# Kernel tuning notes

Measured on AMD Instinct MI355X. Metric: run time of the kernel, lower is better.

## Reference

```python
import jax, jax.numpy as jnp
import numpy as np

# Static module config (matches init_kwargs)
K = 9            # kernel_size for piecewise-linear basis with kernel_shape (3,4)
GROUPS = 1
NLAT_IN, NLON_IN = 361, 720
NLAT_OUT, NLON_OUT = 181, 360
NNZ = 120000


def _disco_s2_contraction(x, ker_idx, row_idx, col_idx, vals):
    """Sparse DISCO contraction: y[b,c,k,ho,wo] = sum_e [ker_e=k][row_e=ho]
    vals_e * x[b,c,hi_e,(wi_e + wo*pscale) % nlon_in].
    Implemented as a longitude-roll scan with gather + segment_sum (no dense psi)."""
    B, C, Hi, Wi = x.shape
    pscale = Wi // NLON_OUT
    hi = col_idx // Wi          # [nnz] input latitude
    wi = col_idx % Wi           # [nnz] input longitude (unshifted)
    seg = ker_idx * NLAT_OUT + row_idx  # [nnz] output (k, ho) segment id

    def step(x_c, _):
        # gather all nnz entries for the current longitude shift: [nnz, B*C]
        g = x_c[:, :, hi, wi].reshape(B * C, -1).T
        y = jax.ops.segment_sum(g * vals[:, None], seg, num_segments=K * NLAT_OUT)
        # roll so next output longitude sees x[..., (wi + pscale) % Wi]
        return jnp.roll(x_c, -pscale, axis=-1), y

    _, ys = jax.lax.scan(step, x, None, length=NLON_OUT)  # [Wo, K*Ho, B*C]
    y = jnp.transpose(ys, (2, 1, 0)).reshape(B, C, K, NLAT_OUT, NLON_OUT)
    return y


def setup_inputs() -> dict:
    key = jax.random.key(0)
    k1, k2, k3, k4, k5, k6, k7 = jax.random.split(key, 7)
    B, Cin, Cout = 1, 32, 32
    x = jax.random.normal(k1, (B, Cin, NLAT_IN, NLON_IN), dtype=jnp.float32)
    psi_ker_idx = jax.random.randint(k2, (NNZ,), 0, K)
    psi_row_idx = jax.random.randint(k3, (NNZ,), 0, NLAT_OUT)
    psi_col_idx = jax.random.randint(k4, (NNZ,), 0, NLAT_IN * NLON_IN)
    psi_vals = jax.random.normal(k5, (NNZ,), dtype=jnp.float32) * 0.05
    groupsize = Cin // GROUPS
    scale = np.sqrt(1.0 / groupsize)
    weight = scale * jax.random.normal(k6, (Cout, groupsize, K), dtype=jnp.float32)
    bias = jax.random.normal(k7, (Cout,), dtype=jnp.float32) * 0.01
    return {"x": x, "psi_ker_idx": psi_ker_idx, "psi_row_idx": psi_row_idx,
            "psi_col_idx": psi_col_idx, "psi_vals": psi_vals,
            "weight": weight, "bias": bias}


def reference(x, psi_ker_idx, psi_row_idx, psi_col_idx, psi_vals, weight, bias):
    # sparse gather-weight-scatter contraction -> [B, C, K, Ho, Wo]
    xk = _disco_s2_contraction(x, psi_ker_idx, psi_row_idx, psi_col_idx, psi_vals)
    B, C, _, H, W = xk.shape
    groupsize = C // GROUPS
    xk = xk.reshape(B, GROUPS, groupsize, K, H, W)
    w = weight.reshape(GROUPS, -1, weight.shape[1], weight.shape[2])  # [g, o, c, k]
    out = jnp.einsum('bgckxy,gock->bgoxy', xk, w).reshape(B, -1, H, W)
    out = out + bias.reshape(1, -1, 1, 1)
    return out
```

## Files before the change

### kernel.cpp

```cpp
#include <hip/hip_runtime.h>
#include <hip/hip_bf16.h>
#include <stdint.h>

typedef uint32_t u32;
typedef unsigned short u16;
typedef float v2f __attribute__((ext_vector_type(2)));

#define NLAT_I 361
#define NLON_I 720
#define NLAT_O 181
#define NLON_O 360
#define KK 9
#define NNZ 120000
#define NSEG (KK * NLAT_O)
#define NPIX (NLAT_O * NLON_O)
#define NCH 32
#define SORT_CAP 512
#define ROWLEN 5760

#define NBLK1 233
#define SEGS_PER_BLK 7
#define NC 8
#define LDSCAP 160
#define SPIN_LIMIT 100

__device__ __forceinline__ u32 f2bf_rne(float f) {
    u32 b = __float_as_uint(f);
    return (b + 0x7FFFu + ((b >> 16) & 1u)) >> 16;
}

__global__ __launch_bounds__(256) void repack_kernel(const float* __restrict__ x,
                                                     u32* __restrict__ xp) {
    __shared__ u16 tile[32][732];
    int hi = blockIdx.x;
    int tid = threadIdx.x;
    const size_t plane = (size_t)NLAT_I * NLON_I;
#pragma unroll 1
    for (int c = 0; c < NCH; c++) {
        for (int col = tid; col < NLON_I; col += 256) {
            tile[c][col] = (u16)f2bf_rne(x[c * plane + (size_t)hi * NLON_I + col]);
        }
    }
    __syncthreads();
    for (int wdx = tid; wdx < 2 * ROWLEN; wdx += 256) {
        int p = wdx / ROWLEN;
        int rem = wdx - p * ROWLEN;
        int j = rem >> 4;
        int cp = rem & 15;
        int col = 2 * j + p;
        u32 v = (u32)tile[2 * cp][col] | ((u32)tile[2 * cp + 1][col] << 16);
        xp[(size_t)(2 * hi + p) * ROWLEN + rem] = v;
    }
}

__global__ __launch_bounds__(256) void hist_kernel(const int* __restrict__ ker,
                                                   const int* __restrict__ row,
                                                   int* __restrict__ counts) {
    int e = blockIdx.x * 256 + threadIdx.x;
    if (e >= NNZ) return;
    int seg = ker[e] * NLAT_O + row[e];
    atomicAdd(&counts[seg], 1);
}

__global__ __launch_bounds__(256) void scan_kernel(const int* __restrict__ counts,
                                                   int* __restrict__ offsets) {
    __shared__ int lsum[256];
    const int CH = 7;
    int t = threadIdx.x;
    int base = t * CH;
    int local[CH];
    int s = 0;
    for (int i = 0; i < CH; i++) {
        int v = (base + i < NSEG) ? counts[base + i] : 0;
        local[i] = s;
        s += v;
    }
    lsum[t] = s;
    __syncthreads();
    for (int off = 1; off < 256; off <<= 1) {
        int v = 0;
        if (t >= off) v = lsum[t - off];
        __syncthreads();
        if (t >= off) lsum[t] += v;
        __syncthreads();
    }
    int pre = (t == 0) ? 0 : lsum[t - 1];
    for (int i = 0; i < CH; i++) {
        if (base + i < NSEG) offsets[base + i] = pre + local[i];
    }
}

__global__ __launch_bounds__(256) void scatter_kernel(const int* __restrict__ ker,
                                                      const int* __restrict__ row,
                                                      const int* __restrict__ col,
                                                      const float* __restrict__ vals,
                                                      const int* __restrict__ offsets,
                                                      int* __restrict__ cursor,
                                                      int2* __restrict__ recs) {
    int e = blockIdx.x * 256 + threadIdx.x;
    if (e >= NNZ) return;
    int seg = ker[e] * NLAT_O + row[e];
    int pos = offsets[seg] + atomicAdd(&cursor[seg], 1);
    int c  = col[e];
    int hi = c / NLON_I;
    int wi = c % NLON_I;
    int p  = wi & 1;
    int a  = wi >> 1;
    u32 meta = ((u32)hi << 10) | ((u32)p << 9) | (u32)a;
    recs[pos] = make_int2((int)meta, __float_as_int(vals[e]));
}

__global__ __launch_bounds__(256) void sort_kernel(const int* __restrict__ offs,
                                                   const int* __restrict__ cnts,
                                                   int2* __restrict__ recs) {
    __shared__ u32 skey[SORT_CAP];
    __shared__ u32 sval[SORT_CAP];
    int s = blockIdx.x;
    int start = offs[s];
    int cnt = cnts[s];
    if (cnt > SORT_CAP) return;
    int t = threadIdx.x;
    for (int i = t; i < cnt; i += 256) {
        int2 r = recs[start + i];
        skey[i] = (u32)r.x;
        sval[i] = (u32)r.y;
    }
    __syncthreads();
    for (int i = t; i < cnt; i += 256) {
        u32 k = skey[i];
        int rank = 0;
        for (int j = 0; j < cnt; j++) {
            u32 kj = skey[j];
            rank += (kj < k || (kj == k && j < i)) ? 1 : 0;
        }
        recs[start + rank] = make_int2((int)k, (int)sval[i]);
    }
}


__device__ __forceinline__ v2f bf2(u32 u) {
    v2f r;
    r.x = __uint_as_float(u << 16);
    r.y = __uint_as_float(u & 0xFFFF0000u);
    return r;
}

__device__ __forceinline__ const uint4* entry_ptr(const u32* __restrict__ xph,
                                                  u32 m, int w) {
    int row = (int)(m >> 9);
    int a   = (int)(m & 0x1FF);
    int idx = a + w;
    idx = (idx >= NLON_O) ? idx - NLON_O : idx;
    return (const uint4*)(xph + ((size_t)(row * NLON_O + idx) << 4));
}

#define FMA8(q0, q1, vv, A)                 \
    {                                       \
        A[0] = bf2(q0.x) * vv + A[0];       \
        A[1] = bf2(q0.y) * vv + A[1];       \
        A[2] = bf2(q0.z) * vv + A[2];       \
        A[3] = bf2(q0.w) * vv + A[3];       \
        A[4] = bf2(q1.x) * vv + A[4];       \
        A[5] = bf2(q1.y) * vv + A[5];       \
        A[6] = bf2(q1.z) * vv + A[6];       \
        A[7] = bf2(q1.w) * vv + A[7];       \
    }

__device__ __forceinline__ void proc_range(const u32* __restrict__ xph,
                                           const int2* __restrict__ rec,
                                           int beg, int end, int w,
                                           v2f* __restrict__ A) {
    int i = beg;
#pragma unroll 1
    for (; i + 4 <= end; i += 4) {
        int2 r0 = rec[i];
        int2 r1 = rec[i + 1];
        int2 r2 = rec[i + 2];
        int2 r3 = rec[i + 3];
        const uint4* p0 = entry_ptr(xph, (u32)r0.x, w);
        const uint4* p1 = entry_ptr(xph, (u32)r1.x, w);
        const uint4* p2 = entry_ptr(xph, (u32)r2.x, w);
        const uint4* p3 = entry_ptr(xph, (u32)r3.x, w);
        uint4 a0 = p0[0]; uint4 a1 = p0[1];
        uint4 b0 = p1[0]; uint4 b1 = p1[1];
        uint4 c0 = p2[0]; uint4 c1 = p2[1];
        uint4 d0 = p3[0]; uint4 d1 = p3[1];
        v2f v0 = {__int_as_float(r0.y), __int_as_float(r0.y)};
        v2f v1 = {__int_as_float(r1.y), __int_as_float(r1.y)};
        v2f v2 = {__int_as_float(r2.y), __int_as_float(r2.y)};
        v2f v3 = {__int_as_float(r3.y), __int_as_float(r3.y)};
        FMA8(a0, a1, v0, A)
        FMA8(b0, b1, v1, A)
        FMA8(c0, c1, v2, A)
        FMA8(d0, d1, v3, A)
    }
#pragma unroll 1
    for (; i < end; ++i) {
        int2 r0 = rec[i];
        const uint4* p0 = entry_ptr(xph, (u32)r0.x, w);
        uint4 a0 = p0[0]; uint4 a1 = p0[1];
        v2f v0 = {__int_as_float(r0.y), __int_as_float(r0.y)};
        FMA8(a0, a1, v0, A)
    }
}

__global__ __launch_bounds__(768, 3) void stage1_kernel(const u32* __restrict__ xp,
                                                        const int* __restrict__ offs,
                                                        const int* __restrict__ cnts,
                                                        const int2* __restrict__ recs,
                                                        int* __restrict__ ctr,
                                                        u16* __restrict__ xk) {
    __shared__ int2 lrec[SEGS_PER_BLK][LDSCAP];
    __shared__ int scnt[SEGS_PER_BLK], soff[SEGS_PER_BLK];

    int b = blockIdx.x;
    int tid = threadIdx.x;

    if (tid < SEGS_PER_BLK) {
        int s = b * SEGS_PER_BLK + tid;
        int ok = (s < NSEG);
        scnt[tid] = ok ? cnts[s] : 0;
        soff[tid] = ok ? offs[s] : 0;
    }
    __syncthreads();

#pragma unroll
    for (int slot = 0; slot < SEGS_PER_BLK; slot++) {
        int c = scnt[slot], o = soff[slot];
        int lim = c < LDSCAP ? c : LDSCAP;
        for (int i = tid; i < lim; i += 768) lrec[slot][i] = recs[o + i];
    }
    __syncthreads();

    int wo = tid >> 1;
    int half = tid & 1;
    bool act = wo < NLON_O;
    int w = act ? wo : 0;
    const u32* xph = xp + half * 8;

    v2f acc[SEGS_PER_BLK][8];
#pragma unroll
    for (int slot = 0; slot < SEGS_PER_BLK; slot++)
#pragma unroll
        for (int j = 0; j < 8; j++) acc[slot][j] = (v2f){0.0f, 0.0f};

    for (int c = 0; c < NC; c++) {
#pragma unroll
        for (int slot = 0; slot < SEGS_PER_BLK; slot++) {
            int cnt = scnt[slot];
            int beg = (c * cnt) / NC;
            int end = ((c + 1) * cnt) / NC;
            if (end <= LDSCAP) {
                proc_range(xph, lrec[slot], beg, end, w, acc[slot]);
            } else {
                proc_range(xph, recs + soff[slot], beg, end, w, acc[slot]);
            }
        }
        if (c < NC - 1) {
            __syncthreads();
            if (tid == 0) {
                __hip_atomic_fetch_add(&ctr[c], 1, __ATOMIC_RELAXED,
                                       __HIP_MEMORY_SCOPE_AGENT);
                int spins = 0;
                while (spins < SPIN_LIMIT &&
                       __hip_atomic_load(&ctr[c], __ATOMIC_RELAXED,
                                         __HIP_MEMORY_SCOPE_AGENT) < (int)gridDim.x) {
                    __builtin_amdgcn_s_sleep(2);
                    ++spins;
                }
            }
            __syncthreads();
        }
    }

    if (act) {
#pragma unroll
        for (int slot = 0; slot < SEGS_PER_BLK; slot++) {
            int s = b * SEGS_PER_BLK + slot;
            if (s < NSEG) {
                int k = s / NLAT_O;
                int ho = s - k * NLAT_O;
                int pix = ho * NLON_O + wo;
#pragma unroll
                for (int j = 0; j < 8; j++) {
                    int ch = half * 16 + 2 * j;
                    xk[(size_t)(ch * KK + k) * NPIX + pix] =
                        (u16)f2bf_rne(acc[slot][j].x);
                    xk[(size_t)((ch + 1) * KK + k) * NPIX + pix] =
                        (u16)f2bf_rne(acc[slot][j].y);
                }
            }
        }
    }
}

__global__ __launch_bounds__(256) void stage2_kernel(const u16* __restrict__ xk,
                                                     const float* __restrict__ W,
                                                     const float* __restrict__ bias,
                                                     float* __restrict__ out) {
    int t = blockIdx.x * 256 + threadIdx.x;
    bool act = t < NPIX / 2;
    int px = act ? t : 0;
    const u32* xk32 = (const u32*)xk;
    float a0[NCH], a1[NCH];
#pragma unroll
    for (int o = 0; o < NCH; o++) { a0[o] = 0.0f; a1[o] = 0.0f; }
#pragma unroll 4
    for (int r = 0; r < NCH * KK; r++) {
        u32 u = xk32[(size_t)r * (NPIX / 2) + px];
        float x0 = __uint_as_float(u << 16);
        float x1 = __uint_as_float(u & 0xFFFF0000u);
#pragma unroll
        for (int o = 0; o < NCH; o++) {
            float wv = W[o * (NCH * KK) + r];
            a0[o] = fmaf(wv, x0, a0[o]);
            a1[o] = fmaf(wv, x1, a1[o]);
        }
    }
    if (act) {
#pragma unroll
        for (int o = 0; o < NCH; o++) {
            float2 v = make_float2(a0[o] + bias[o], a1[o] + bias[o]);
            *(float2*)(out + (size_t)o * NPIX + 2 * t) = v;
        }
    }
}

extern "C" void kernel_launch(void* const* d_in, const int* in_sizes, int n_in,
                              void* d_out, int out_size, void* d_ws, size_t ws_size,
                              hipStream_t stream) {
    const float* x    = (const float*)d_in[0];
    const int* ker    = (const int*)d_in[1];
    const int* row    = (const int*)d_in[2];
    const int* col    = (const int*)d_in[3];
    const float* vals = (const float*)d_in[4];
    const float* W    = (const float*)d_in[5];
    const float* bias = (const float*)d_in[6];
    float* out        = (float*)d_out;

    char* ws = (char*)d_ws;
    const size_t off_xp   = 0;
    const size_t sz_xp    = (size_t)NLAT_I * 2 * ROWLEN * 4;
    const size_t off_cnt  = off_xp + sz_xp;
    const size_t off_off  = off_cnt + 6528;
    const size_t off_cur  = off_off + 6528;
    const size_t off_ctr  = off_cur + 6528;
    const size_t off_rec  = off_ctr + 64;
    const size_t off_xk   = off_rec + (size_t)NNZ * 8;

    u32* xp      = (u32*)(ws + off_xp);
    int* counts  = (int*)(ws + off_cnt);
    int* offsets = (int*)(ws + off_off);
    int* cursor  = (int*)(ws + off_cur);
    int* ctr     = (int*)(ws + off_ctr);
    int2* recs   = (int2*)(ws + off_rec);
    u16* xk      = (u16*)(ws + off_xk);

    hipMemsetAsync(ws + off_cnt, 0, 3 * 6528 + 64, stream);

    repack_kernel<<<NLAT_I, 256, 0, stream>>>(x, xp);
    hist_kernel<<<(NNZ + 255) / 256, 256, 0, stream>>>(ker, row, counts);
    scan_kernel<<<1, 256, 0, stream>>>(counts, offsets);
    scatter_kernel<<<(NNZ + 255) / 256, 256, 0, stream>>>(ker, row, col, vals,
                                                          offsets, cursor, recs);
    sort_kernel<<<NSEG, 256, 0, stream>>>(offsets, counts, recs);
    stage1_kernel<<<NBLK1, 768, 0, stream>>>(xp, offsets, counts, recs, ctr, xk);
    stage2_kernel<<<(NPIX / 2 + 255) / 256, 256, 0, stream>>>(xk, W, bias, out);
}
```

Measured before the change: 410.6 us.

## Stream whole input rows into an LDS ring via async global-to-LDS loads

Stage1 now precomputes a flat list of the input rows each nonzero touches. It prefetches each full repacked row (23 KB) into a 4-deep LDS ring buffer using global_load_lds, three entries ahead. Each nonzero is then processed by all threads reading swizzled LDS slots instead of doing scattered per-thread global gathers, at the cost of a block-wide barrier per nonzero. Overflow entries beyond LDSCAP move to a separate global-gather tail loop after the main pipeline. The larger shared-memory footprint may lower occupancy below the launch-bounds target of 3 blocks.

```diff
diff --git a/kernel.cpp b/kernel.cpp
--- a/kernel.cpp
+++ b/kernel.cpp
@@ -17,6 +17,8 @@
 #define NCH 32
 #define SORT_CAP 512
 #define ROWLEN 5760
+#define ROWBYTES 23040
+#define ROWCHUNK 1440
 
 #define NBLK1 233
 #define SEGS_PER_BLK 7
@@ -24,10 +26,15 @@
 #define LDSCAP 160
 #define SPIN_LIMIT 100
 
+#define AS1 __attribute__((address_space(1)))
+#define AS3 __attribute__((address_space(3)))
+
 __device__ __forceinline__ u32 f2bf_rne(float f) {
     u32 b = __float_as_uint(f);
     return (b + 0x7FFFu + ((b >> 16) & 1u)) >> 16;
 }
+
+__device__ __forceinline__ int imin(int a, int b) { return a < b ? a : b; }
 
 __global__ __launch_bounds__(256) void repack_kernel(const float* __restrict__ x,
                                                      u32* __restrict__ xp) {
@@ -138,22 +145,6 @@
 }
 
 
-__device__ __forceinline__ v2f bf2(u32 u) {
-    v2f r;
-    r.x = __uint_as_float(u << 16);
-    r.y = __uint_as_float(u & 0xFFFF0000u);
-    return r;
-}
-
-__device__ __forceinline__ const uint4* entry_ptr(const u32* __restrict__ xph,
-                                                  u32 m, int w) {
-    int row = (int)(m >> 9);
-    int a   = (int)(m & 0x1FF);
-    int idx = a + w;
-    idx = (idx >= NLON_O) ? idx - NLON_O : idx;
-    return (const uint4*)(xph + ((size_t)(row * NLON_O + idx) << 4));
-}
-
 #define FMA8(q0, q1, vv, A)                 \
     {                                       \
         A[0] = bf2(q0.x) * vv + A[0];       \
@@ -166,42 +157,11 @@
         A[7] = bf2(q1.w) * vv + A[7];       \
     }
 
-__device__ __forceinline__ void proc_range(const u32* __restrict__ xph,
-                                           const int2* __restrict__ rec,
-                                           int beg, int end, int w,
-                                           v2f* __restrict__ A) {
-    int i = beg;
-#pragma unroll 1
-    for (; i + 4 <= end; i += 4) {
-        int2 r0 = rec[i];
-        int2 r1 = rec[i + 1];
-        int2 r2 = rec[i + 2];
-        int2 r3 = rec[i + 3];
-        const uint4* p0 = entry_ptr(xph, (u32)r0.x, w);
-        const uint4* p1 = entry_ptr(xph, (u32)r1.x, w);
-        const uint4* p2 = entry_ptr(xph, (u32)r2.x, w);
-        const uint4* p3 = entry_ptr(xph, (u32)r3.x, w);
-        uint4 a0 = p0[0]; uint4 a1 = p0[1];
-        uint4 b0 = p1[0]; uint4 b1 = p1[1];
-        uint4 c0 = p2[0]; uint4 c1 = p2[1];
-        uint4 d0 = p3[0]; uint4 d1 = p3[1];
-        v2f v0 = {__int_as_float(r0.y), __int_as_float(r0.y)};
-        v2f v1 = {__int_as_float(r1.y), __int_as_float(r1.y)};
-        v2f v2 = {__int_as_float(r2.y), __int_as_float(r2.y)};
-        v2f v3 = {__int_as_float(r3.y), __int_as_float(r3.y)};
-        FMA8(a0, a1, v0, A)
-        FMA8(b0, b1, v1, A)
-        FMA8(c0, c1, v2, A)
-        FMA8(d0, d1, v3, A)
-    }
-#pragma unroll 1
-    for (; i < end; ++i) {
-        int2 r0 = rec[i];
-        const uint4* p0 = entry_ptr(xph, (u32)r0.x, w);
-        uint4 a0 = p0[0]; uint4 a1 = p0[1];
-        v2f v0 = {__int_as_float(r0.y), __int_as_float(r0.y)};
-        FMA8(a0, a1, v0, A)
-    }
+__device__ __forceinline__ v2f bf2(u32 u) {
+    v2f r;
+    r.x = __uint_as_float(u << 16);
+    r.y = __uint_as_float(u & 0xFFFF0000u);
+    return r;
 }
 
 __global__ __launch_bounds__(768, 3) void stage1_kernel(const u32* __restrict__ xp,
@@ -210,11 +170,17 @@
                                                         const int2* __restrict__ recs,
                                                         int* __restrict__ ctr,
                                                         u16* __restrict__ xk) {
+    __shared__ uint4 ring4[4][ROWCHUNK];
     __shared__ int2 lrec[SEGS_PER_BLK][LDSCAP];
-    __shared__ int scnt[SEGS_PER_BLK], soff[SEGS_PER_BLK];
+    __shared__ u32 frow[SEGS_PER_BLK * LDSCAP + 8];
+    __shared__ int scnt[8], soff[8];
+    __shared__ int cbase[NC][SEGS_PER_BLK];
+    __shared__ int s_tot;
 
     int b = blockIdx.x;
     int tid = threadIdx.x;
+    int lane = tid & 63;
+    int wv = tid >> 6;
 
     if (tid < SEGS_PER_BLK) {
         int s = b * SEGS_PER_BLK + tid;
@@ -226,17 +192,46 @@
 
 #pragma unroll
     for (int slot = 0; slot < SEGS_PER_BLK; slot++) {
-        int c = scnt[slot], o = soff[slot];
-        int lim = c < LDSCAP ? c : LDSCAP;
-        for (int i = tid; i < lim; i += 768) lrec[slot][i] = recs[o + i];
-    }
-    __syncthreads();
-
-    int wo = tid >> 1;
-    int half = tid & 1;
+        int c = imin(scnt[slot], LDSCAP);
+        int o = soff[slot];
+        for (int i = tid; i < c; i += 768) lrec[slot][i] = recs[o + i];
+    }
+    __syncthreads();
+
+    if (tid == 0) {
+        int g = 0;
+        for (int c = 0; c < NC; c++)
+            for (int slot = 0; slot < SEGS_PER_BLK; slot++) {
+                cbase[c][slot] = g;
+                int cc = imin(scnt[slot], LDSCAP);
+                g += ((c + 1) * cc) / NC - (c * cc) / NC;
+            }
+        s_tot = g;
+        frow[g] = 0; frow[g + 1] = 0; frow[g + 2] = 0;
+    }
+    __syncthreads();
+    if (tid < NC * SEGS_PER_BLK) {
+        int c = tid / SEGS_PER_BLK, slot = tid % SEGS_PER_BLK;
+        int cc = imin(scnt[slot], LDSCAP);
+        int beg = (c * cc) / NC, end = ((c + 1) * cc) / NC;
+        int base = cbase[c][slot];
+        for (int i = beg; i < end; i++)
+            frow[base + (i - beg)] = ((u32)lrec[slot][i].x) >> 9;
+    }
+    __syncthreads();
+    int tot = s_tot;
+
+    int wo = tid >> 1, h = tid & 1;
     bool act = wo < NLON_O;
     int w = act ? wo : 0;
-    const u32* xph = xp + half * 8;
+    const char* xpb = (const char*)xp;
+
+    int sl0 = wv * 120 + lane;
+    int sl1 = wv * 120 + 64 + lane;
+    size_t goff0 = (size_t)((sl0 & ~7) | ((sl0 - (sl0 >> 3)) & 7)) * 16;
+    size_t goff1 = (size_t)((sl1 & ~7) | ((sl1 - (sl1 >> 3)) & 7)) * 16;
+    bool lane1ok = lane < 56;
+    int wvb = wv * 120;
 
     v2f acc[SEGS_PER_BLK][8];
 #pragma unroll
@@ -244,16 +239,56 @@
 #pragma unroll
         for (int j = 0; j < 8; j++) acc[slot][j] = (v2f){0.0f, 0.0f};
 
+#pragma unroll
+    for (int r = 0; r < 3; r++) {
+        const char* rb = xpb + (size_t)frow[r] * ROWBYTES;
+        __builtin_amdgcn_global_load_lds((const AS1 void*)(rb + goff0),
+                                         (AS3 void*)&ring4[r][wvb], 16, 0, 0);
+        if (lane1ok)
+            __builtin_amdgcn_global_load_lds((const AS1 void*)(rb + goff1),
+                                             (AS3 void*)&ring4[r][wvb + 64], 16, 0, 0);
+    }
+
+    int g = 0;
     for (int c = 0; c < NC; c++) {
 #pragma unroll
         for (int slot = 0; slot < SEGS_PER_BLK; slot++) {
-            int cnt = scnt[slot];
-            int beg = (c * cnt) / NC;
-            int end = ((c + 1) * cnt) / NC;
-            if (end <= LDSCAP) {
-                proc_range(xph, lrec[slot], beg, end, w, acc[slot]);
-            } else {
-                proc_range(xph, recs + soff[slot], beg, end, w, acc[slot]);
+            int cc = imin(scnt[slot], LDSCAP);
+            int beg = (c * cc) / NC;
+            int end = ((c + 1) * cc) / NC;
+#pragma unroll 1
+            for (int i = beg; i < end; i++) {
+                asm volatile("s_waitcnt vmcnt(4)" ::: "memory");
+                __builtin_amdgcn_s_barrier();
+                asm volatile("" ::: "memory");
+                __builtin_amdgcn_sched_barrier(0);
+
+                int2 r = lrec[slot][i];
+                int a = r.x & 0x1FF;
+                float vf = __int_as_float(r.y);
+                v2f vv = {vf, vf};
+                int idx = a + w;
+                idx = (idx >= NLON_O) ? idx - NLON_O : idx;
+                int c0 = (idx << 2) + (h << 1);
+                int bb = c0 >> 3;
+                int t0 = c0 + bb;
+                int s0 = (c0 & ~7) | (t0 & 7);
+                int s1 = (c0 & ~7) | ((t0 + 1) & 7);
+                const uint4* rb4 = &ring4[g & 3][0];
+                uint4 q0 = rb4[s0];
+                uint4 q1 = rb4[s1];
+                FMA8(q0, q1, vv, acc[slot])
+
+                u32 nrow = frow[g + 3];
+                const char* nb = xpb + (size_t)nrow * ROWBYTES;
+                int buf = (g + 3) & 3;
+                __builtin_amdgcn_global_load_lds((const AS1 void*)(nb + goff0),
+                                                 (AS3 void*)&ring4[buf][wvb], 16, 0, 0);
+                if (lane1ok)
+                    __builtin_amdgcn_global_load_lds((const AS1 void*)(nb + goff1),
+                                                     (AS3 void*)&ring4[buf][wvb + 64],
+                                                     16, 0, 0);
+                g++;
             }
         }
         if (c < NC - 1) {
@@ -273,6 +308,30 @@
         }
     }
 
+#pragma unroll
+    for (int slot = 0; slot < SEGS_PER_BLK; slot++) {
+        int cnt = scnt[slot];
+        if (cnt > LDSCAP) {
+            const int2* rg = recs + soff[slot];
+            const u32* xph = xp + h * 8;
+#pragma unroll 1
+            for (int i = LDSCAP; i < cnt; i++) {
+                int2 r0 = rg[i];
+                u32 m0 = (u32)r0.x;
+                float vf = __int_as_float(r0.y);
+                v2f vv = {vf, vf};
+                int row0 = (int)(m0 >> 9);
+                int a0 = (int)(m0 & 0x1FF);
+                int idx0 = a0 + w;
+                idx0 = (idx0 >= NLON_O) ? idx0 - NLON_O : idx0;
+                const uint4* rp = (const uint4*)(xph + ((size_t)(row0 * NLON_O + idx0) << 4));
+                uint4 q0 = rp[0];
+                uint4 q1 = rp[1];
+                FMA8(q0, q1, vv, acc[slot])
+            }
+        }
+    }
+
     if (act) {
 #pragma unroll
         for (int slot = 0; slot < SEGS_PER_BLK; slot++) {
@@ -283,7 +342,7 @@
                 int pix = ho * NLON_O + wo;
 #pragma unroll
                 for (int j = 0; j < 8; j++) {
-                    int ch = half * 16 + 2 * j;
+                    int ch = h * 16 + 2 * j;
                     xk[(size_t)(ch * KK + k) * NPIX + pix] =
                         (u16)f2bf_rne(acc[slot][j].x);
                     xk[(size_t)((ch + 1) * KK + k) * NPIX + pix] =
```

Measured after the change: 499.1 us. 21.6% more time.

## Software-pipeline gather loads in stage1 and reduce channel chunk count

Applied to the files above, without the earlier changes.

Rewrites the inner gather-FMA loop as a two-stage software pipeline: the next pair of record gathers is issued while the previous pair is being accumulated, with odd and tail entries handled separately. This is meant to hide global/LDS gather latency behind FMA work. It also lowers the number of chunks per segment (NC from 8 to 6), so there are fewer sync/spin rounds per block, each with more work. The pipelined version keeps more registers live, which under the 768-thread, 3-blocks-per-SM launch bounds could cause spills.

```diff
diff --git a/kernel.cpp b/kernel.cpp
--- a/kernel.cpp
+++ b/kernel.cpp
@@ -20,7 +20,7 @@
 
 #define NBLK1 233
 #define SEGS_PER_BLK 7
-#define NC 8
+#define NC 6
 #define LDSCAP 160
 #define SPIN_LIMIT 100
 
@@ -28,6 +28,8 @@
     u32 b = __float_as_uint(f);
     return (b + 0x7FFFu + ((b >> 16) & 1u)) >> 16;
 }
+
+__device__ __forceinline__ int imin(int a, int b) { return a < b ? a : b; }
 
 __global__ __launch_bounds__(256) void repack_kernel(const float* __restrict__ x,
                                                      u32* __restrict__ xp) {
@@ -166,41 +168,79 @@
         A[7] = bf2(q1.w) * vv + A[7];       \
     }
 
+#define DECLP(X) uint4 X##q0, X##q1, X##q2, X##q3; v2f X##v0, X##v1;
+
+#define LOADP(X, rec, i)                                        \
+    {                                                           \
+        int2 r0_ = (rec)[(i)];                                  \
+        int2 r1_ = (rec)[(i) + 1];                              \
+        float f0_ = __int_as_float(r0_.y);                      \
+        float f1_ = __int_as_float(r1_.y);                      \
+        X##v0 = (v2f){f0_, f0_};                                \
+        X##v1 = (v2f){f1_, f1_};                                \
+        const uint4* p0_ = entry_ptr(xph, (u32)r0_.x, w);       \
+        const uint4* p1_ = entry_ptr(xph, (u32)r1_.x, w);       \
+        X##q0 = p0_[0];                                         \
+        X##q1 = p0_[1];                                         \
+        X##q2 = p1_[0];                                         \
+        X##q3 = p1_[1];                                         \
+    }
+
+#define CONSP(X, A)                                             \
+    {                                                           \
+        FMA8(X##q0, X##q1, X##v0, A)                            \
+        FMA8(X##q2, X##q3, X##v1, A)                            \
+    }
+
+__device__ __forceinline__ void proc_single(const u32* __restrict__ xph,
+                                            const int2* __restrict__ rec,
+                                            int i, int w, v2f* __restrict__ A) {
+    int2 r0 = rec[i];
+    float vf = __int_as_float(r0.y);
+    v2f vv = {vf, vf};
+    const uint4* p0 = entry_ptr(xph, (u32)r0.x, w);
+    uint4 q0 = p0[0];
+    uint4 q1 = p0[1];
+    FMA8(q0, q1, vv, A)
+}
+
 __device__ __forceinline__ void proc_range(const u32* __restrict__ xph,
                                            const int2* __restrict__ rec,
                                            int beg, int end, int w,
                                            v2f* __restrict__ A) {
-    int i = beg;
+    int n = end - beg;
+    if (n <= 0) return;
+    if (n & 1) {
+        proc_single(xph, rec, beg, w, A);
+        beg++;
+        n--;
+    }
+    if (n <= 0) return;
+    DECLP(Pa)
+    DECLP(Pb)
+    if (n >= 4) {
+        LOADP(Pa, rec, beg)
+        LOADP(Pb, rec, beg + 2)
+        int i = beg + 4;
 #pragma unroll 1
-    for (; i + 4 <= end; i += 4) {
-        int2 r0 = rec[i];
-        int2 r1 = rec[i + 1];
-        int2 r2 = rec[i + 2];
-        int2 r3 = rec[i + 3];
-        const uint4* p0 = entry_ptr(xph, (u32)r0.x, w);
-        const uint4* p1 = entry_ptr(xph, (u32)r1.x, w);
-        const uint4* p2 = entry_ptr(xph, (u32)r2.x, w);
-        const uint4* p3 = entry_ptr(xph, (u32)r3.x, w);
-        uint4 a0 = p0[0]; uint4 a1 = p0[1];
-        uint4 b0 = p1[0]; uint4 b1 = p1[1];
-        uint4 c0 = p2[0]; uint4 c1 = p2[1];
-        uint4 d0 = p3[0]; uint4 d1 = p3[1];
-        v2f v0 = {__int_as_float(r0.y), __int_as_float(r0.y)};
-        v2f v1 = {__int_as_float(r1.y), __int_as_float(r1.y)};
-        v2f v2 = {__int_as_float(r2.y), __int_as_float(r2.y)};
-        v2f v3 = {__int_as_float(r3.y), __int_as_float(r3.y)};
-        FMA8(a0, a1, v0, A)
-        FMA8(b0, b1, v1, A)
-        FMA8(c0, c1, v2, A)
-        FMA8(d0, d1, v3, A)
-    }
-#pragma unroll 1
-    for (; i < end; ++i) {
-        int2 r0 = rec[i];
-        const uint4* p0 = entry_ptr(xph, (u32)r0.x, w);
-        uint4 a0 = p0[0]; uint4 a1 = p0[1];
-        v2f v0 = {__int_as_float(r0.y), __int_as_float(r0.y)};
-        FMA8(a0, a1, v0, A)
+        for (; i + 4 <= end; i += 4) {
+            CONSP(Pa, A)
+            LOADP(Pa, rec, i)
+            CONSP(Pb, A)
+            LOADP(Pb, rec, i + 2)
+        }
+        if (i < end) {
+            CONSP(Pa, A)
+            LOADP(Pa, rec, i)
+            CONSP(Pb, A)
+            CONSP(Pa, A)
+        } else {
+            CONSP(Pa, A)
+            CONSP(Pb, A)
+        }
+    } else {
+        LOADP(Pa, rec, beg)
+        CONSP(Pa, A)
     }
 }
 
@@ -226,17 +266,16 @@
 
 #pragma unroll
     for (int slot = 0; slot < SEGS_PER_BLK; slot++) {
-        int c = scnt[slot], o = soff[slot];
-        int lim = c < LDSCAP ? c : LDSCAP;
-        for (int i = tid; i < lim; i += 768) lrec[slot][i] = recs[o + i];
+        int c = imin(scnt[slot], LDSCAP);
+        int o = soff[slot];
+        for (int i = tid; i < c; i += 768) lrec[slot][i] = recs[o + i];
     }
     __syncthreads();
 
-    int wo = tid >> 1;
-    int half = tid & 1;
+    int wo = tid >> 1, h = tid & 1;
     bool act = wo < NLON_O;
     int w = act ? wo : 0;
-    const u32* xph = xp + half * 8;
+    const u32* xph = xp + h * 8;
 
     v2f acc[SEGS_PER_BLK][8];
 #pragma unroll
@@ -283,7 +322,7 @@
                 int pix = ho * NLON_O + wo;
 #pragma unroll
                 for (int j = 0; j < 8; j++) {
-                    int ch = half * 16 + 2 * j;
+                    int ch = h * 16 + 2 * j;
                     xk[(size_t)(ch * KK + k) * NPIX + pix] =
                         (u16)f2bf_rne(acc[slot][j].x);
                     xk[(size_t)((ch + 1) * KK + k) * NPIX + pix] =
```

After: 561.2 us. 1.37x slower.

## Split stage2 reduction dimension across four thread slices with LDS reduce

Applied to the files above, without the earlier changes.

Stage2 now assigns 64 pixel-pairs per block and splits the 288-long channel×kernel reduction into four slices of 72, one per 64-thread group. Partial sums are combined through shared memory, with each slice writing a quarter of the output channels. This gives four times as many blocks (about 510 instead of 128), to fill the GPU's compute units better on a small grid, at the cost of LDS traffic and barriers. Stage1's chunk count NC also drops from 8 to 4, which halves its synchronization rounds.

```diff
diff --git a/kernel.cpp b/kernel.cpp
--- a/kernel.cpp
+++ b/kernel.cpp
@@ -20,7 +20,7 @@
 
 #define NBLK1 233
 #define SEGS_PER_BLK 7
-#define NC 8
+#define NC 4
 #define LDSCAP 160
 #define SPIN_LIMIT 100
 
@@ -28,6 +28,8 @@
     u32 b = __float_as_uint(f);
     return (b + 0x7FFFu + ((b >> 16) & 1u)) >> 16;
 }
+
+__device__ __forceinline__ int imin(int a, int b) { return a < b ? a : b; }
 
 __global__ __launch_bounds__(256) void repack_kernel(const float* __restrict__ x,
                                                      u32* __restrict__ xp) {
@@ -226,17 +228,16 @@
 
 #pragma unroll
     for (int slot = 0; slot < SEGS_PER_BLK; slot++) {
-        int c = scnt[slot], o = soff[slot];
-        int lim = c < LDSCAP ? c : LDSCAP;
-        for (int i = tid; i < lim; i += 768) lrec[slot][i] = recs[o + i];
+        int c = imin(scnt[slot], LDSCAP);
+        int o = soff[slot];
+        for (int i = tid; i < c; i += 768) lrec[slot][i] = recs[o + i];
     }
     __syncthreads();
 
-    int wo = tid >> 1;
-    int half = tid & 1;
+    int wo = tid >> 1, h = tid & 1;
     bool act = wo < NLON_O;
     int w = act ? wo : 0;
-    const u32* xph = xp + half * 8;
+    const u32* xph = xp + h * 8;
 
     v2f acc[SEGS_PER_BLK][8];
 #pragma unroll
@@ -283,7 +284,7 @@
                 int pix = ho * NLON_O + wo;
 #pragma unroll
                 for (int j = 0; j < 8; j++) {
-                    int ch = half * 16 + 2 * j;
+                    int ch = h * 16 + 2 * j;
                     xk[(size_t)(ch * KK + k) * NPIX + pix] =
                         (u16)f2bf_rne(acc[slot][j].x);
                     xk[(size_t)((ch + 1) * KK + k) * NPIX + pix] =
@@ -294,19 +295,29 @@
     }
 }
 
+#define S2_PP 64
+#define S2_RPK 72
+
 __global__ __launch_bounds__(256) void stage2_kernel(const u16* __restrict__ xk,
                                                      const float* __restrict__ W,
                                                      const float* __restrict__ bias,
                                                      float* __restrict__ out) {
-    int t = blockIdx.x * 256 + threadIdx.x;
-    bool act = t < NPIX / 2;
-    int px = act ? t : 0;
+    __shared__ float2 red[4][S2_PP][17];
+    int pp  = threadIdx.x & 63;
+    int ksl = threadIdx.x >> 6;
+    int px2 = blockIdx.x * S2_PP + pp;
+    bool act = px2 < NPIX / 2;
+    int px = act ? px2 : 0;
     const u32* xk32 = (const u32*)xk;
+
     float a0[NCH], a1[NCH];
 #pragma unroll
     for (int o = 0; o < NCH; o++) { a0[o] = 0.0f; a1[o] = 0.0f; }
+
+    int rbase = ksl * S2_RPK;
 #pragma unroll 4
-    for (int r = 0; r < NCH * KK; r++) {
+    for (int rr = 0; rr < S2_RPK; rr++) {
+        int r = rbase + rr;
         u32 u = xk32[(size_t)r * (NPIX / 2) + px];
         float x0 = __uint_as_float(u << 16);
         float x1 = __uint_as_float(u & 0xFFFF0000u);
@@ -317,11 +328,31 @@
             a1[o] = fmaf(wv, x1, a1[o]);
         }
     }
-    if (act) {
-#pragma unroll
-        for (int o = 0; o < NCH; o++) {
-            float2 v = make_float2(a0[o] + bias[o], a1[o] + bias[o]);
-            *(float2*)(out + (size_t)o * NPIX + 2 * t) = v;
+
+#pragma unroll 1
+    for (int half = 0; half < 2; half++) {
+        __syncthreads();
+#pragma unroll
+        for (int j = 0; j < 16; j++) {
+            int o = half * 16 + j;
+            red[ksl][pp][j] = make_float2(a0[o], a1[o]);
+        }
+        __syncthreads();
+#pragma unroll
+        for (int j = 0; j < 4; j++) {
+            int oo = ksl * 4 + j;
+            float2 s0 = red[0][pp][oo];
+            float2 s1 = red[1][pp][oo];
+            float2 s2 = red[2][pp][oo];
+            float2 s3 = red[3][pp][oo];
+            float sx = s0.x + s1.x + s2.x + s3.x;
+            float sy = s0.y + s1.y + s2.y + s3.y;
+            int o = half * 16 + oo;
+            if (act) {
+                float bv = bias[o];
+                float2 v = make_float2(sx + bv, sy + bv);
+                *(float2*)(out + (size_t)o * NPIX + 2 * px2) = v;
+            }
         }
     }
 }
@@ -365,5 +396,5 @@
                                                           offsets, cursor, recs);
     sort_kernel<<<NSEG, 256, 0, stream>>>(offsets, counts, recs);
     stage1_kernel<<<NBLK1, 768, 0, stream>>>(xp, offsets, counts, recs, ctr, xk);
-    stage2_kernel<<<(NPIX / 2 + 255) / 256, 256, 0, stream>>>(xk, W, bias, out);
-}
+    stage2_kernel<<<(NPIX / 2 + S2_PP - 1) / S2_PP, 256, 0, stream>>>(xk, W, bias, out);
+}
```

Result: faster. 339.3 us (-17.4%).
